# Optimization experiments

Measured on AMD Instinct MI355X. Metric: run time of the kernel, lower is better.

## Reference

```python
import jax, jax.numpy as jnp
import numpy as np

TEMPERATURE = 1.0 / 13.544


def setup_inputs() -> dict:
    key = jax.random.key(0)
    x = jax.random.normal(key, (8, 2048, 128), dtype=jnp.float32)
    return {"x": x, "is_batch_mode": 1}


def reference(x, is_batch_mode):
    # batched pairwise squared-L2 distance via norm expansion:
    # d[b,i,j] = ||x_i||^2 - 2 x_i . x_j + ||x_j||^2
    sq = jnp.sum(x * x, axis=-1)                       # [B, N]
    dots = jnp.einsum('bnd,bmd->bnm', x, x)            # [B, N, N]
    dist = sq[:, :, None] - 2.0 * dots + sq[:, None, :]
    dist = jnp.maximum(dist, 0.0)
    sim = jax.nn.softmax(-TEMPERATURE * dist, axis=-1)  # [B, N, N]
    return sim[..., None]                               # [B, N, N, 1]
```

## Files before the change

kernel.cpp:

```cpp
#include <hip/hip_runtime.h>
#include <hip/hip_bf16.h>
#include <cstdint>


using bf16x8 = __attribute__((ext_vector_type(8))) short;
using f32x4  = __attribute__((ext_vector_type(4))) float;

#define TEMP   (1.0f / 13.544f)
#define LOG2E  1.4426950408889634f

#define GLOBAL_AS __attribute__((address_space(1)))
#define LDS_AS    __attribute__((address_space(3)))

__global__ __launch_bounds__(256) void prep_kernel(
    const float* __restrict__ x, uint4* __restrict__ xbf, float* __restrict__ csq)
{
    const int t   = threadIdx.x;
    const int lr  = t >> 4;
    const int q   = t & 15;
    const int row = blockIdx.x * 16 + lr;

    const float* xp = x + (size_t)row * 128 + q * 8;
    float4 a0 = *(const float4*)(xp);
    float4 a1 = *(const float4*)(xp + 4);
    float v[8] = {a0.x, a0.y, a0.z, a0.w, a1.x, a1.y, a1.z, a1.w};

    unsigned u[8];
    float s = 0.f;
#pragma unroll
    for (int e = 0; e < 8; ++e) {
        unsigned ui = __float_as_uint(v[e]);
        unsigned r  = (ui + 0x7FFFu + ((ui >> 16) & 1u)) >> 16;
        u[e] = r;
        float d = __uint_as_float(r << 16);
        s += d * d;
    }
    uint4 pack;
    pack.x = u[0] | (u[1] << 16);
    pack.y = u[2] | (u[3] << 16);
    pack.z = u[4] | (u[5] << 16);
    pack.w = u[6] | (u[7] << 16);

    const int b  = row >> 11;
    const int g  = (row >> 4) & 127;
    const int rr = row & 15;
    xbf[(b * 128 + g) * 256 + q * 16 + rr] = pack;

#pragma unroll
    for (int m = 1; m < 16; m <<= 1) s += __shfl_xor(s, m, 64);
    if (q == 0) csq[row] = s * (-TEMP * LOG2E);
}

__global__ __launch_bounds__(256, 2) void sim_kernel(
    const uint4* __restrict__ xbf, const float* __restrict__ csq, float* __restrict__ out)
{
    const int blk  = blockIdx.x;
    const int b    = blk >> 7;
    const int i0   = (blk & 127) * 16;
    const int tid  = threadIdx.x;
    const int w    = tid >> 6;
    const int lane = tid & 63;
    const int quad = lane >> 4;
    const int l15  = lane & 15;

    __shared__ __align__(16) ushort lsB[16384];
    __shared__ float lsSum[4][16];
    __shared__ __align__(16) float lsInv[16];

    const uint4* xbb  = xbf + (size_t)b * (128 * 256);
    const float* csqb = csq + b * 2048;

    bf16x8 afrag[4];
#pragma unroll
    for (int k4 = 0; k4 < 4; ++k4) {
        uint4 vv = xbb[(i0 >> 4) * 256 + (k4 * 4 + quad) * 16 + l15];
        afrag[k4] = __builtin_bit_cast(bf16x8, vv);
    }

    float csqi[4];
    {
        float4 vv = *(const float4*)(csqb + i0 + quad * 4);
        csqi[0] = vv.x; csqi[1] = vv.y; csqi[2] = vv.z; csqi[3] = vv.w;
    }

    const float C2L = 2.0f * TEMP * LOG2E;
    const int   c0  = w * 32;

    float P[16][2][4];
    float sum_[4] = {};

#pragma unroll
    for (int jt = 0; jt < 16; ++jt) {
        const int j0 = jt * 128;
        __syncthreads();
        {
            const uint4* src = xbb + (j0 >> 4) * 256 + w * 512 + lane;
#pragma unroll
            for (int it = 0; it < 8; ++it) {
                __builtin_amdgcn_global_load_lds(
                    (const GLOBAL_AS void*)(src + it * 64),
                    (LDS_AS void*)(&lsB[w * 4096 + it * 512]),
                    16, 0, 0);
            }
        }
        __syncthreads();

        const float csqj0 = csqb[j0 + c0 + l15];
        const float csqj1 = csqb[j0 + c0 + 16 + l15];

        f32x4 acc[2] = {};
#pragma unroll
        for (int k4 = 0; k4 < 4; ++k4) {
            const int qq = k4 * 4 + quad;
            bf16x8 b0 = *(const bf16x8*)(&lsB[(w * 2 + 0) * 2048 + qq * 128 + l15 * 8]);
            bf16x8 b1 = *(const bf16x8*)(&lsB[(w * 2 + 1) * 2048 + qq * 128 + l15 * 8]);
            acc[0] = __builtin_amdgcn_mfma_f32_16x16x32_bf16(afrag[k4], b0, acc[0], 0, 0, 0);
            acc[1] = __builtin_amdgcn_mfma_f32_16x16x32_bf16(afrag[k4], b1, acc[1], 0, 0, 0);
        }

#pragma unroll
        for (int n = 0; n < 2; ++n) {
            const float cj = n ? csqj1 : csqj0;
#pragma unroll
            for (int r = 0; r < 4; ++r) {
                float lg = fminf(fmaf(C2L, acc[n][r], csqi[r] + cj), 0.f);
                float p  = exp2f(lg);
                P[jt][n][r] = p;
                sum_[r] += p;
            }
        }
    }

#pragma unroll
    for (int r = 0; r < 4; ++r) {
        float s = sum_[r];
        s += __shfl_xor(s, 1, 64);
        s += __shfl_xor(s, 2, 64);
        s += __shfl_xor(s, 4, 64);
        s += __shfl_xor(s, 8, 64);
        sum_[r] = s;
    }
    if (l15 == 0) {
#pragma unroll
        for (int r = 0; r < 4; ++r) lsSum[w][quad * 4 + r] = sum_[r];
    }
    __syncthreads();
    if (tid < 16) {
        float tot = lsSum[0][tid] + lsSum[1][tid] + lsSum[2][tid] + lsSum[3][tid];
        lsInv[tid] = 1.0f / tot;
    }
    __syncthreads();

    float inv_[4];
    {
        float4 vv = *(const float4*)(&lsInv[quad * 4]);
        inv_[0] = vv.x; inv_[1] = vv.y; inv_[2] = vv.z; inv_[3] = vv.w;
    }

    float* outrow = out + ((size_t)b * 2048 + i0) * 2048;
#pragma unroll
    for (int jt = 0; jt < 16; ++jt) {
#pragma unroll
        for (int r = 0; r < 4; ++r) {
            float* op = outrow + (size_t)(quad * 4 + r) * 2048 + jt * 128 + c0 + l15;
            op[0]  = P[jt][0][r] * inv_[r];
            op[16] = P[jt][1][r] * inv_[r];
        }
    }
}

extern "C" void kernel_launch(void* const* d_in, const int* in_sizes, int n_in,
                              void* d_out, int out_size, void* d_ws, size_t ws_size,
                              hipStream_t stream) {
    const float* x   = (const float*)d_in[0];
    float*       out = (float*)d_out;
    uint4* xbf = (uint4*)d_ws;
    float* csq = (float*)((char*)d_ws + (size_t)4 * 1024 * 1024);

    prep_kernel<<<1024, 256, 0, stream>>>(x, xbf, csq);
    sim_kernel<<<1024, 256, 0, stream>>>(xbf, csq, out);
}
```

Measured before the change: 170.2 us.

## Store probabilities as packed fp16, drop LDS staging, raise occupancy, interleave batches

The unnormalized softmax numerators are now held as packed fp16 pairs instead of fp32, which halves the register footprint and allows three blocks per CU instead of two. The LDS staging of the B tiles and the two barriers per tile are removed, so each wave loads its B fragments directly from global memory. Block-to-batch mapping is changed so consecutive blocks cover different batches, and the store loop order is swapped. Rounding the numerators to fp16 with round-toward-zero adds relative error of about 1e-3 to the output, and very small probabilities may underflow to zero.

```diff
diff --git a/kernel.cpp b/kernel.cpp
--- a/kernel.cpp
+++ b/kernel.cpp
@@ -5,12 +5,10 @@
 
 using bf16x8 = __attribute__((ext_vector_type(8))) short;
 using f32x4  = __attribute__((ext_vector_type(4))) float;
+using half2v = __attribute__((ext_vector_type(2))) __fp16;
 
 #define TEMP   (1.0f / 13.544f)
 #define LOG2E  1.4426950408889634f
-
-#define GLOBAL_AS __attribute__((address_space(1)))
-#define LDS_AS    __attribute__((address_space(3)))
 
 __global__ __launch_bounds__(256) void prep_kernel(
     const float* __restrict__ x, uint4* __restrict__ xbf, float* __restrict__ csq)
@@ -18,7 +16,7 @@
     const int t   = threadIdx.x;
     const int lr  = t >> 4;
     const int q   = t & 15;
-    const int row = blockIdx.x * 16 + lr;
+    const int row = (blockIdx.x & 7) * 2048 + (blockIdx.x >> 3) * 16 + lr;
 
     const float* xp = x + (size_t)row * 128 + q * 8;
     float4 a0 = *(const float4*)(xp);
@@ -51,19 +49,18 @@
     if (q == 0) csq[row] = s * (-TEMP * LOG2E);
 }
 
-__global__ __launch_bounds__(256, 2) void sim_kernel(
+__global__ __launch_bounds__(256, 3) void sim_kernel(
     const uint4* __restrict__ xbf, const float* __restrict__ csq, float* __restrict__ out)
 {
     const int blk  = blockIdx.x;
-    const int b    = blk >> 7;
-    const int i0   = (blk & 127) * 16;
+    const int b    = blk & 7;
+    const int i0   = (blk >> 3) * 16;
     const int tid  = threadIdx.x;
     const int w    = tid >> 6;
     const int lane = tid & 63;
     const int quad = lane >> 4;
     const int l15  = lane & 15;
 
-    __shared__ __align__(16) ushort lsB[16384];
     __shared__ float lsSum[4][16];
     __shared__ __align__(16) float lsInv[16];
 
@@ -86,48 +83,38 @@
     const float C2L = 2.0f * TEMP * LOG2E;
     const int   c0  = w * 32;
 
-    float P[16][2][4];
-    float sum_[4] = {};
+    half2v P[16][4];
+    float  sum_[4] = {};
 
 #pragma unroll
     for (int jt = 0; jt < 16; ++jt) {
-        const int j0 = jt * 128;
-        __syncthreads();
-        {
-            const uint4* src = xbb + (j0 >> 4) * 256 + w * 512 + lane;
-#pragma unroll
-            for (int it = 0; it < 8; ++it) {
-                __builtin_amdgcn_global_load_lds(
-                    (const GLOBAL_AS void*)(src + it * 64),
-                    (LDS_AS void*)(&lsB[w * 4096 + it * 512]),
-                    16, 0, 0);
-            }
-        }
-        __syncthreads();
-
-        const float csqj0 = csqb[j0 + c0 + l15];
-        const float csqj1 = csqb[j0 + c0 + 16 + l15];
-
-        f32x4 acc[2] = {};
+        const uint4* bg = xbb + (jt * 8 + w * 2) * 256;
+        uint4 b0[4], b1[4];
 #pragma unroll
         for (int k4 = 0; k4 < 4; ++k4) {
-            const int qq = k4 * 4 + quad;
-            bf16x8 b0 = *(const bf16x8*)(&lsB[(w * 2 + 0) * 2048 + qq * 128 + l15 * 8]);
-            bf16x8 b1 = *(const bf16x8*)(&lsB[(w * 2 + 1) * 2048 + qq * 128 + l15 * 8]);
-            acc[0] = __builtin_amdgcn_mfma_f32_16x16x32_bf16(afrag[k4], b0, acc[0], 0, 0, 0);
-            acc[1] = __builtin_amdgcn_mfma_f32_16x16x32_bf16(afrag[k4], b1, acc[1], 0, 0, 0);
+            b0[k4] = bg[(k4 * 4 + quad) * 16 + l15];
+            b1[k4] = bg[256 + (k4 * 4 + quad) * 16 + l15];
+        }
+        const float csqj0 = csqb[jt * 128 + c0 + l15];
+        const float csqj1 = csqb[jt * 128 + c0 + 16 + l15];
+
+        f32x4 acc0 = {}, acc1 = {};
+#pragma unroll
+        for (int k4 = 0; k4 < 4; ++k4) {
+            acc0 = __builtin_amdgcn_mfma_f32_16x16x32_bf16(
+                       afrag[k4], __builtin_bit_cast(bf16x8, b0[k4]), acc0, 0, 0, 0);
+            acc1 = __builtin_amdgcn_mfma_f32_16x16x32_bf16(
+                       afrag[k4], __builtin_bit_cast(bf16x8, b1[k4]), acc1, 0, 0, 0);
         }
 
 #pragma unroll
-        for (int n = 0; n < 2; ++n) {
-            const float cj = n ? csqj1 : csqj0;
-#pragma unroll
-            for (int r = 0; r < 4; ++r) {
-                float lg = fminf(fmaf(C2L, acc[n][r], csqi[r] + cj), 0.f);
-                float p  = exp2f(lg);
-                P[jt][n][r] = p;
-                sum_[r] += p;
-            }
+        for (int r = 0; r < 4; ++r) {
+            float lg0 = fminf(fmaf(C2L, acc0[r], csqi[r] + csqj0), 0.f);
+            float lg1 = fminf(fmaf(C2L, acc1[r], csqi[r] + csqj1), 0.f);
+            float p0  = exp2f(lg0);
+            float p1  = exp2f(lg1);
+            sum_[r] += p0 + p1;
+            P[jt][r] = __builtin_amdgcn_cvt_pkrtz(p0, p1);
         }
     }
 
@@ -159,12 +146,12 @@
 
     float* outrow = out + ((size_t)b * 2048 + i0) * 2048;
 #pragma unroll
-    for (int jt = 0; jt < 16; ++jt) {
+    for (int r = 0; r < 4; ++r) {
+        float* op = outrow + (size_t)(quad * 4 + r) * 2048 + c0 + l15;
 #pragma unroll
-        for (int r = 0; r < 4; ++r) {
-            float* op = outrow + (size_t)(quad * 4 + r) * 2048 + jt * 128 + c0 + l15;
-            op[0]  = P[jt][0][r] * inv_[r];
-            op[16] = P[jt][1][r] * inv_[r];
+        for (int jt = 0; jt < 16; ++jt) {
+            op[jt * 128]      = (float)P[jt][r].x * inv_[r];
+            op[jt * 128 + 16] = (float)P[jt][r].y * inv_[r];
         }
     }
 }
```

Result: slower. 209.7 us (+23.2%).
